# Performance work log

Hardware: AMD Instinct MI355X
Metric: run time of the kernel (lower is better)

Reference implementation:

```python
import jax, jax.numpy as jnp
import numpy as np

BS, FH, FW, NA = 32, 100, 100, 9
IMG_H, IMG_W = 1600, 1600
STRIDE = 16
KEEP_PRE, KEEP_POST, NMS_THR = 1000, 300, 0.7


def _grid_anchors():
    scales = np.array([128.0, 256.0, 512.0])
    ratios = np.array([0.5, 1.0, 2.0])
    ws, hs = [], []
    for s in scales:
        for r in ratios:
            ws.append(s * np.sqrt(1.0 / r))
            hs.append(s * np.sqrt(r))
    ws, hs = np.array(ws), np.array(hs)  # [9]
    sx = (np.arange(FW) + 0.5) * STRIDE
    sy = (np.arange(FH) + 0.5) * STRIDE
    cx, cy = np.meshgrid(sx, sy)  # [FH,FW]
    cx = cx.reshape(-1, 1)
    cy = cy.reshape(-1, 1)
    anchors = np.stack([
        cx - 0.5 * ws, cy - 0.5 * hs, cx + 0.5 * ws, cy + 0.5 * hs
    ], axis=-1).reshape(-1, 4)  # [FH*FW*NA, 4]
    return anchors.astype(np.float32)


def setup_inputs() -> dict:
    key = jax.random.key(0)
    k1, k2 = jax.random.split(key)
    N = FH * FW * NA
    cls_logits = jax.random.normal(k1, (BS, N, 1), dtype=jnp.float32)
    reg_deltas = jax.random.normal(k2, (BS, N, 4), dtype=jnp.float32) * 0.3
    anchors = jnp.asarray(_grid_anchors())
    return {"cls_logits": cls_logits, "reg_deltas": reg_deltas,
            "anchors": anchors, "img_h": IMG_H, "img_w": IMG_W}


def _offsets2boxes(deltas, anchors):
    # deltas: [bs,N,4] (dx,dy,dw,dh); anchors: [N,4] xyxy
    aw = anchors[:, 2] - anchors[:, 0]
    ah = anchors[:, 3] - anchors[:, 1]
    acx = anchors[:, 0] + 0.5 * aw
    acy = anchors[:, 1] + 0.5 * ah
    cx = deltas[..., 0] * aw + acx
    cy = deltas[..., 1] * ah + acy
    w = jnp.exp(deltas[..., 2]) * aw
    h = jnp.exp(deltas[..., 3]) * ah
    return jnp.stack([cx - 0.5 * w, cy - 0.5 * h, cx + 0.5 * w, cy + 0.5 * h], axis=-1)


def _iou_matrix(b):
    # b: [K,4] -> [K,K]
    area = (b[:, 2] - b[:, 0]) * (b[:, 3] - b[:, 1])
    lt = jnp.maximum(b[:, None, :2], b[None, :, :2])
    rb = jnp.minimum(b[:, None, 2:], b[None, :, 2:])
    wh = jnp.clip(rb - lt, 0.0)
    inter = wh[..., 0] * wh[..., 1]
    return inter / (area[:, None] + area[None, :] - inter + 1e-12)


def _detect_single(boxes, scores, img_h, img_w):
    # boxes: [N,4], scores: [N]
    top_scores, idx = jax.lax.top_k(scores, KEEP_PRE)
    b = boxes[idx]  # [K,4], already score-sorted descending
    b = jnp.stack([
        jnp.clip(b[:, 0], 0.0, img_w), jnp.clip(b[:, 1], 0.0, img_h),
        jnp.clip(b[:, 2], 0.0, img_w), jnp.clip(b[:, 3], 0.0, img_h)
    ], axis=-1)
    iou = _iou_matrix(b)  # [K,K]
    K = KEEP_PRE
    cols = jnp.arange(K)

    def body(i, keep):
        # if box i still kept, suppress later boxes with IoU > thr (greedy NMS)
        sup = keep[i] & (iou[i] > NMS_THR) & (cols > i)
        return keep & ~sup

    keep = jax.lax.fori_loop(0, K, body, jnp.ones((K,), dtype=bool))
    # kept boxes first (stable sort preserves descending-score order), take top P
    order = jnp.argsort(~keep, stable=True)[:KEEP_POST]
    valid = keep[order]
    det = jnp.concatenate([b[order], top_scores[order, None]], axis=-1)
    return det * valid[:, None].astype(det.dtype)  # padded rows zeroed


def reference(cls_logits, reg_deltas, anchors, img_h, img_w):
    bs = cls_logits.shape[0]
    scores = jax.nn.sigmoid(cls_logits.reshape(bs, -1))  # [bs,N]
    boxes = _offsets2boxes(reg_deltas.reshape(bs, -1, 4), anchors)  # [bs,N,4]
    fh = jnp.float32(img_h)
    fw = jnp.float32(img_w)
    dets = jax.vmap(lambda b, s: _detect_single(b, s, fh, fw))(boxes, scores)
    return dets  # [bs, KEEP_POST, 5] (xmin,ymin,xmax,ymax,score), zero-padded
```

## Files before the change

### kernel.cpp

```cpp
#include <hip/hip_runtime.h>
#include <stdint.h>

#pragma clang fp contract(off)

#define BS 32
#define NANCH 90000
#define KEEP_PRE 1000
#define KEEP_POST 300
#define NMS_THR 0.7f
#define NBINS 4096
#define CAND_MAX 4096
#define MW 16
#define CNT_STRIDE 32
#define NSLICE 8

typedef unsigned long long u64;
typedef unsigned int u32;

#define HIST_BYTES ((size_t)BS * NBINS * 4)
#define CNT_OFF    (HIST_BYTES)
#define CNT_BYTES  ((size_t)BS * CNT_STRIDE * 4)
#define BTHR_OFF   (CNT_OFF + CNT_BYTES)
#define CAND_OFF   (BTHR_OFF + 128)
#define BOX_OFF    (CAND_OFF + (size_t)BS * CAND_MAX * 8)
#define SCORE_OFF  (BOX_OFF + (size_t)BS * KEEP_PRE * 16)
#define MASK_OFF   (SCORE_OFF + (size_t)BS * KEEP_PRE * 4)

__device__ __forceinline__ u32 fmono(float f) {
    u32 u = __float_as_uint(f);
    return (u & 0x80000000u) ? ~u : (u | 0x80000000u);
}

__global__ __launch_bounds__(256) void hist_kernel(const float* __restrict__ logits,
                                                   u32* __restrict__ hist) {
    __shared__ u32 lh[NBINS];
    const int b = blockIdx.y;
    for (int i = threadIdx.x; i < NBINS; i += 256) lh[i] = 0;
    __syncthreads();
    const float* src = logits + (size_t)b * NANCH;
    const int stride = 256 * gridDim.x;
    for (int i = blockIdx.x * 256 + threadIdx.x; i < NANCH; i += stride) {
        u32 m = fmono(src[i]);
        atomicAdd(&lh[m >> 20], 1u);
    }
    __syncthreads();
    u32* gh = hist + (size_t)b * NBINS;
    for (int i = threadIdx.x; i < NBINS; i += 256)
        if (lh[i]) atomicAdd(&gh[i], lh[i]);
}

__global__ __launch_bounds__(256) void thresh_kernel(const u32* __restrict__ hist,
                                                     u32* __restrict__ Bthr) {
    __shared__ u32 part[256];
    const int b = blockIdx.x;
    const u32* h = hist + (size_t)b * NBINS;
    u32 s = 0;
    for (int k = 0; k < 16; k++) s += h[threadIdx.x * 16 + k];
    part[threadIdx.x] = s;
    __syncthreads();
    if (threadIdx.x == 0) {
        u32 cum = 0;
        int c = 255;
        for (; c >= 0; c--) {
            if (cum + part[c] >= KEEP_PRE) break;
            cum += part[c];
        }
        if (c < 0) c = 0;
        int bin = c * 16 + 15;
        for (; bin >= c * 16; bin--) {
            if (cum + h[bin] >= KEEP_PRE) break;
            cum += h[bin];
        }
        if (bin < c * 16) bin = c * 16;
        Bthr[b] = (u32)bin;
    }
}

__global__ __launch_bounds__(256) void compact_kernel(const float* __restrict__ logits,
                                                      const u32* __restrict__ Bthr,
                                                      u32* __restrict__ cnt,
                                                      u64* __restrict__ cand) {
    const int b = blockIdx.y;
    const int i = blockIdx.x * 256 + threadIdx.x;
    __shared__ u32 blk_cnt;
    __shared__ u32 blk_base;
    if (threadIdx.x == 0) blk_cnt = 0;
    __syncthreads();
    bool is_cand = false;
    u32 m = 0;
    if (i < NANCH) {
        m = fmono(logits[(size_t)b * NANCH + i]);
        is_cand = (m >> 20) >= Bthr[b];
    }
    u64 ballot = __ballot(is_cand);
    const u32 lane = threadIdx.x & 63;
    u32 wbase = 0;
    u32 old = 0;
    if (ballot) {
        if (lane == 0) old = atomicAdd(&blk_cnt, (u32)__popcll(ballot));
        wbase = __shfl(old, 0);
    }
    __syncthreads();
    if (threadIdx.x == 0 && blk_cnt)
        blk_base = atomicAdd(&cnt[b * CNT_STRIDE], blk_cnt);
    __syncthreads();
    if (is_cand) {
        u32 prefix = (u32)__popcll(ballot & ((1ull << lane) - 1ull));
        u32 pos = blk_base + wbase + prefix;
        if (pos < CAND_MAX)
            cand[(size_t)b * CAND_MAX + pos] = ((u64)m << 32) | (u32)(~(u32)i);
    }
}

__global__ __launch_bounds__(256) void select_kernel(const float* __restrict__ deltas,
                                                     const float* __restrict__ anchors,
                                                     const u32* __restrict__ cnt,
                                                     const u64* __restrict__ cand,
                                                     float4* __restrict__ selbox,
                                                     float* __restrict__ selscore,
                                                     const int* __restrict__ p_img_h,
                                                     const int* __restrict__ p_img_w) {
    __shared__ u64 keys[CAND_MAX];
    const int b = blockIdx.y;
    const int slice = blockIdx.x;
    const int n = (int)min(cnt[b * CNT_STRIDE], (u32)CAND_MAX);
    const u64* src = cand + (size_t)b * CAND_MAX;
    for (int i = threadIdx.x; i < n; i += 256)
        keys[i] = src[i];
    __syncthreads();
    const int per = (n + NSLICE - 1) / NSLICE;
    const int i0 = slice * per;
    const int i1 = min(i0 + per, n);
    const float W = (float)(*p_img_w);
    const float H = (float)(*p_img_h);
    const float4* d4 = (const float4*)deltas;
    const float4* a4 = (const float4*)anchors;
    for (int i = i0 + threadIdx.x; i < i1; i += 256) {
        const u64 me = keys[i];
        int rank = 0;
        int j = 0;
        for (; j + 16 <= n; j += 16) {
            int r0 = 0;
#pragma unroll
            for (int k = 0; k < 16; k++) r0 += (keys[j + k] > me);
            rank += r0;
        }
        for (; j < n; j++) rank += (keys[j] > me);
        if (rank < KEEP_PRE) {
            u32 idx = ~(u32)me;
            u32 m = (u32)(me >> 32);
            u32 ub = (m & 0x80000000u) ? (m ^ 0x80000000u) : ~m;
            float logit = __uint_as_float(ub);
            float score = 1.0f / (1.0f + expf(-logit));
            float4 d = d4[(size_t)b * NANCH + idx];
            float4 a = a4[idx];
            float aw = a.z - a.x, ah = a.w - a.y;
            float acx = a.x + 0.5f * aw, acy = a.y + 0.5f * ah;
            float cx = d.x * aw + acx, cy = d.y * ah + acy;
            float w = expf(d.z) * aw, h = expf(d.w) * ah;
            float x1 = cx - 0.5f * w, y1 = cy - 0.5f * h;
            float x2 = cx + 0.5f * w, y2 = cy + 0.5f * h;
            x1 = fminf(fmaxf(x1, 0.0f), W); y1 = fminf(fmaxf(y1, 0.0f), H);
            x2 = fminf(fmaxf(x2, 0.0f), W); y2 = fminf(fmaxf(y2, 0.0f), H);
            selbox[(size_t)b * KEEP_PRE + rank] = make_float4(x1, y1, x2, y2);
            selscore[(size_t)b * KEEP_PRE + rank] = score;
        }
    }
}

__global__ __launch_bounds__(256) void iou_kernel(const float4* __restrict__ selbox,
                                                  u64* __restrict__ mask) {
    const int b = blockIdx.y;
    const int w = blockIdx.x & 15;
    const int chunk = blockIdx.x >> 4;
    const int i = chunk * 256 + threadIdx.x;
    __shared__ float4 cb[64];
    __shared__ float ca[64];
    if (threadIdx.x < 64) {
        int j = w * 64 + threadIdx.x;
        float4 bx = (j < KEEP_PRE) ? selbox[(size_t)b * KEEP_PRE + j]
                                   : make_float4(0, 0, 0, 0);
        cb[threadIdx.x] = bx;
        ca[threadIdx.x] = (bx.z - bx.x) * (bx.w - bx.y);
    }
    __syncthreads();
    if (i >= KEEP_PRE) return;
    float4 bi = selbox[(size_t)b * KEEP_PRE + i];
    float ai = (bi.z - bi.x) * (bi.w - bi.y);
    u64 bits = 0;
    const int jbase = w * 64;
    for (int jj = 0; jj < 64; jj++) {
        int j = jbase + jj;
        if (j > i && j < KEEP_PRE) {
            float4 bj = cb[jj];
            float ltx = fmaxf(bi.x, bj.x), lty = fmaxf(bi.y, bj.y);
            float rbx = fminf(bi.z, bj.z), rby = fminf(bi.w, bj.w);
            float wx = fmaxf(rbx - ltx, 0.0f), wy = fmaxf(rby - lty, 0.0f);
            float inter = wx * wy;
            float denom = ai + ca[jj] - inter + 1e-12f;
            if (inter / denom > NMS_THR) bits |= (1ull << jj);
        }
    }
    mask[((size_t)b * KEEP_PRE + i) * MW + w] = bits;
}

#define CH_ROWS 64
#define CH_WORDS (CH_ROWS * MW)
#define NCHUNK ((KEEP_PRE + CH_ROWS - 1) / CH_ROWS)

__global__ __launch_bounds__(256) void nms_out_kernel(const u64* __restrict__ mask,
                                                      const float4* __restrict__ selbox,
                                                      const float* __restrict__ selscore,
                                                      float* __restrict__ out) {
    const int b = blockIdx.x;
    __shared__ u64 lbuf[2][CH_WORDS];
    __shared__ u64 keepw[MW];
    __shared__ u32 wpre[MW + 1];
    __shared__ int ls_stop;
    const int tid = threadIdx.x;
    const u64* mrow = mask + (size_t)b * KEEP_PRE * MW;

    auto load_chunk = [&](int c) {
        int idx = tid - 128;
        if (idx < 0) return;
        const int words = (c == NCHUNK - 1)
                            ? (KEEP_PRE - (NCHUNK - 1) * CH_ROWS) * MW
                            : CH_WORDS;
        const u64* gsrc = mrow + (size_t)c * CH_WORDS;
        u64* dst = lbuf[c & 1];
#pragma unroll
        for (int k = 0; k < 4; k++) {
            int off = k * 256 + idx * 2;
            ulonglong2 v;
            if (off < words) v = *(const ulonglong2*)(gsrc + off);
            else { v.x = 0ull; v.y = 0ull; }
            *(ulonglong2*)(dst + off) = v;
        }
    };

    if (tid == 0) ls_stop = 0;
    load_chunk(0);
    __syncthreads();

    u64 remv = 0;
    int kept_total = 0;
    const int lw = tid & 15;
    for (int c = 0; c < NCHUNK; c++) {
        if (c + 1 < NCHUNK) load_chunk(c + 1);
        if (tid < 64) {
            const u64* lb = lbuf[c & 1];
            u64 cur = __shfl(remv, c);
#pragma unroll
            for (int blk = 0; blk < 8; blk++) {
                u64 R[8], rwv[8];
#pragma unroll
                for (int k = 0; k < 8; k++)
                    R[k] = lb[(size_t)(blk * 8 + k) * MW + lw];
#pragma unroll
                for (int k = 0; k < 8; k++)
                    rwv[k] = lb[(size_t)(blk * 8 + k) * MW + c];
#pragma unroll
                for (int k = 0; k < 8; k++) {
                    const int p = blk * 8 + k;
                    u64 msk = ((cur >> p) & 1ull) ? 0ull : ~0ull;
                    remv |= R[k] & msk;
                    cur  |= rwv[k] & msk;
                }
            }
            kept_total += 64 - (int)__popcll(cur);
            if (c + 1 < NCHUNK && kept_total >= KEEP_POST) {
                if (lw > c) remv = ~0ull;
                if (tid == 0) ls_stop = 1;
            }
        }
        __syncthreads();
        if (ls_stop) break;
    }

    if (tid < MW) {
        u64 kw = ~remv;
        if (tid == MW - 1) kw &= (1ull << (KEEP_PRE - 64 * (MW - 1))) - 1ull;
        keepw[tid] = kw;
    }
    __syncthreads();
    if (tid == 0) {
        u32 cnt = 0;
        for (int w = 0; w < MW; w++) { wpre[w] = cnt; cnt += (u32)__popcll(keepw[w]); }
        wpre[MW] = cnt;
    }
    __syncthreads();
    const int total = (int)wpre[MW];
    float* outb = out + (size_t)b * KEEP_POST * 5;
    for (int i = tid; i < KEEP_PRE; i += 256) {
        int w = i >> 6;
        u64 kw = keepw[w];
        if ((kw >> (i & 63)) & 1ull) {
            int rank = (int)wpre[w] + __popcll(kw & ((1ull << (i & 63)) - 1ull));
            if (rank < KEEP_POST) {
                float4 bx = selbox[(size_t)b * KEEP_PRE + i];
                float sc = selscore[(size_t)b * KEEP_PRE + i];
                outb[rank * 5 + 0] = bx.x;
                outb[rank * 5 + 1] = bx.y;
                outb[rank * 5 + 2] = bx.z;
                outb[rank * 5 + 3] = bx.w;
                outb[rank * 5 + 4] = sc;
            }
        }
    }
    for (int r = tid; r < KEEP_POST; r += 256) {
        if (r >= total) {
            outb[r * 5 + 0] = 0.0f;
            outb[r * 5 + 1] = 0.0f;
            outb[r * 5 + 2] = 0.0f;
            outb[r * 5 + 3] = 0.0f;
            outb[r * 5 + 4] = 0.0f;
        }
    }
}

extern "C" void kernel_launch(void* const* d_in, const int* in_sizes, int n_in,
                              void* d_out, int out_size, void* d_ws, size_t ws_size,
                              hipStream_t stream) {
    const float* logits  = (const float*)d_in[0];
    const float* deltas  = (const float*)d_in[1];
    const float* anchors = (const float*)d_in[2];
    const int* p_img_h   = (const int*)d_in[3];
    const int* p_img_w   = (const int*)d_in[4];

    char* ws = (char*)d_ws;
    u32* hist     = (u32*)(ws);
    u32* cnt      = (u32*)(ws + CNT_OFF);
    u32* Bthr     = (u32*)(ws + BTHR_OFF);
    u64* cand     = (u64*)(ws + CAND_OFF);
    float4* selbox = (float4*)(ws + BOX_OFF);
    float* selscore = (float*)(ws + SCORE_OFF);
    u64* mask     = (u64*)(ws + MASK_OFF);

    hipMemsetAsync(ws, 0, CNT_OFF + CNT_BYTES, stream);

    hist_kernel<<<dim3(16, BS), 256, 0, stream>>>(logits, hist);
    thresh_kernel<<<BS, 256, 0, stream>>>(hist, Bthr);
    compact_kernel<<<dim3((NANCH + 255) / 256, BS), 256, 0, stream>>>(logits, Bthr, cnt, cand);
    select_kernel<<<dim3(NSLICE, BS), 256, 0, stream>>>(deltas, anchors, cnt, cand,
                                                        selbox, selscore, p_img_h, p_img_w);
    iou_kernel<<<dim3(64, BS), 256, 0, stream>>>(selbox, mask);
    nms_out_kernel<<<BS, 256, 0, stream>>>(mask, selbox, selscore, (float*)d_out);
}
```

Before: 187.0 us.

## Fuse RPN proposal pipeline into a single cooperative kernel with grid syncs

Replaces the memset and six separate kernel launches (histogram, threshold, compaction, rank-select, IoU mask, NMS/output) with one cooperative kernel of 256 blocks that uses grid.sync between stages. This removes per-launch overhead and inter-kernel gaps, and the stages share a union of shared-memory buffers. In exchange, the compaction and IoU stages now run on 256 blocks instead of thousands, serialising more work per block. Grid-wide barriers also carry their own cost, and several stages leave most blocks idle.

```diff
diff --git a/kernel.cpp b/kernel.cpp
--- a/kernel.cpp
+++ b/kernel.cpp
@@ -1,5 +1,8 @@
 #include <hip/hip_runtime.h>
+#include <hip/hip_cooperative_groups.h>
 #include <stdint.h>
+
+namespace cg = cooperative_groups;
 
 #pragma clang fp contract(off)
 
@@ -13,6 +16,7 @@
 #define MW 16
 #define CNT_STRIDE 32
 #define NSLICE 8
+#define SLICE_N 11250
 
 typedef unsigned long long u64;
 typedef unsigned int u32;
@@ -26,294 +30,310 @@
 #define SCORE_OFF  (BOX_OFF + (size_t)BS * KEEP_PRE * 16)
 #define MASK_OFF   (SCORE_OFF + (size_t)BS * KEEP_PRE * 4)
 
+#define CH_ROWS 64
+#define CH_WORDS (CH_ROWS * MW)
+#define NCHUNK ((KEEP_PRE + CH_ROWS - 1) / CH_ROWS)
+
 __device__ __forceinline__ u32 fmono(float f) {
     u32 u = __float_as_uint(f);
     return (u & 0x80000000u) ? ~u : (u | 0x80000000u);
 }
 
-__global__ __launch_bounds__(256) void hist_kernel(const float* __restrict__ logits,
-                                                   u32* __restrict__ hist) {
-    __shared__ u32 lh[NBINS];
-    const int b = blockIdx.y;
-    for (int i = threadIdx.x; i < NBINS; i += 256) lh[i] = 0;
-    __syncthreads();
-    const float* src = logits + (size_t)b * NANCH;
-    const int stride = 256 * gridDim.x;
-    for (int i = blockIdx.x * 256 + threadIdx.x; i < NANCH; i += stride) {
-        u32 m = fmono(src[i]);
-        atomicAdd(&lh[m >> 20], 1u);
-    }
-    __syncthreads();
-    u32* gh = hist + (size_t)b * NBINS;
-    for (int i = threadIdx.x; i < NBINS; i += 256)
-        if (lh[i]) atomicAdd(&gh[i], lh[i]);
-}
-
-__global__ __launch_bounds__(256) void thresh_kernel(const u32* __restrict__ hist,
-                                                     u32* __restrict__ Bthr) {
-    __shared__ u32 part[256];
-    const int b = blockIdx.x;
-    const u32* h = hist + (size_t)b * NBINS;
-    u32 s = 0;
-    for (int k = 0; k < 16; k++) s += h[threadIdx.x * 16 + k];
-    part[threadIdx.x] = s;
-    __syncthreads();
-    if (threadIdx.x == 0) {
-        u32 cum = 0;
-        int c = 255;
-        for (; c >= 0; c--) {
-            if (cum + part[c] >= KEEP_PRE) break;
-            cum += part[c];
-        }
-        if (c < 0) c = 0;
-        int bin = c * 16 + 15;
-        for (; bin >= c * 16; bin--) {
-            if (cum + h[bin] >= KEEP_PRE) break;
-            cum += h[bin];
-        }
-        if (bin < c * 16) bin = c * 16;
-        Bthr[b] = (u32)bin;
-    }
-}
-
-__global__ __launch_bounds__(256) void compact_kernel(const float* __restrict__ logits,
-                                                      const u32* __restrict__ Bthr,
-                                                      u32* __restrict__ cnt,
-                                                      u64* __restrict__ cand) {
-    const int b = blockIdx.y;
-    const int i = blockIdx.x * 256 + threadIdx.x;
-    __shared__ u32 blk_cnt;
-    __shared__ u32 blk_base;
-    if (threadIdx.x == 0) blk_cnt = 0;
-    __syncthreads();
-    bool is_cand = false;
-    u32 m = 0;
-    if (i < NANCH) {
-        m = fmono(logits[(size_t)b * NANCH + i]);
-        is_cand = (m >> 20) >= Bthr[b];
-    }
-    u64 ballot = __ballot(is_cand);
-    const u32 lane = threadIdx.x & 63;
-    u32 wbase = 0;
-    u32 old = 0;
-    if (ballot) {
-        if (lane == 0) old = atomicAdd(&blk_cnt, (u32)__popcll(ballot));
-        wbase = __shfl(old, 0);
-    }
-    __syncthreads();
-    if (threadIdx.x == 0 && blk_cnt)
-        blk_base = atomicAdd(&cnt[b * CNT_STRIDE], blk_cnt);
-    __syncthreads();
-    if (is_cand) {
-        u32 prefix = (u32)__popcll(ballot & ((1ull << lane) - 1ull));
-        u32 pos = blk_base + wbase + prefix;
-        if (pos < CAND_MAX)
-            cand[(size_t)b * CAND_MAX + pos] = ((u64)m << 32) | (u32)(~(u32)i);
-    }
-}
-
-__global__ __launch_bounds__(256) void select_kernel(const float* __restrict__ deltas,
-                                                     const float* __restrict__ anchors,
-                                                     const u32* __restrict__ cnt,
-                                                     const u64* __restrict__ cand,
-                                                     float4* __restrict__ selbox,
-                                                     float* __restrict__ selscore,
-                                                     const int* __restrict__ p_img_h,
-                                                     const int* __restrict__ p_img_w) {
-    __shared__ u64 keys[CAND_MAX];
-    const int b = blockIdx.y;
-    const int slice = blockIdx.x;
-    const int n = (int)min(cnt[b * CNT_STRIDE], (u32)CAND_MAX);
-    const u64* src = cand + (size_t)b * CAND_MAX;
-    for (int i = threadIdx.x; i < n; i += 256)
-        keys[i] = src[i];
-    __syncthreads();
-    const int per = (n + NSLICE - 1) / NSLICE;
-    const int i0 = slice * per;
-    const int i1 = min(i0 + per, n);
-    const float W = (float)(*p_img_w);
-    const float H = (float)(*p_img_h);
-    const float4* d4 = (const float4*)deltas;
-    const float4* a4 = (const float4*)anchors;
-    for (int i = i0 + threadIdx.x; i < i1; i += 256) {
-        const u64 me = keys[i];
-        int rank = 0;
-        int j = 0;
-        for (; j + 16 <= n; j += 16) {
-            int r0 = 0;
-#pragma unroll
-            for (int k = 0; k < 16; k++) r0 += (keys[j + k] > me);
-            rank += r0;
-        }
-        for (; j < n; j++) rank += (keys[j] > me);
-        if (rank < KEEP_PRE) {
-            u32 idx = ~(u32)me;
-            u32 m = (u32)(me >> 32);
-            u32 ub = (m & 0x80000000u) ? (m ^ 0x80000000u) : ~m;
-            float logit = __uint_as_float(ub);
-            float score = 1.0f / (1.0f + expf(-logit));
-            float4 d = d4[(size_t)b * NANCH + idx];
-            float4 a = a4[idx];
-            float aw = a.z - a.x, ah = a.w - a.y;
-            float acx = a.x + 0.5f * aw, acy = a.y + 0.5f * ah;
-            float cx = d.x * aw + acx, cy = d.y * ah + acy;
-            float w = expf(d.z) * aw, h = expf(d.w) * ah;
-            float x1 = cx - 0.5f * w, y1 = cy - 0.5f * h;
-            float x2 = cx + 0.5f * w, y2 = cy + 0.5f * h;
-            x1 = fminf(fmaxf(x1, 0.0f), W); y1 = fminf(fmaxf(y1, 0.0f), H);
-            x2 = fminf(fmaxf(x2, 0.0f), W); y2 = fminf(fmaxf(y2, 0.0f), H);
-            selbox[(size_t)b * KEEP_PRE + rank] = make_float4(x1, y1, x2, y2);
-            selscore[(size_t)b * KEEP_PRE + rank] = score;
-        }
-    }
-}
-
-__global__ __launch_bounds__(256) void iou_kernel(const float4* __restrict__ selbox,
-                                                  u64* __restrict__ mask) {
-    const int b = blockIdx.y;
-    const int w = blockIdx.x & 15;
-    const int chunk = blockIdx.x >> 4;
-    const int i = chunk * 256 + threadIdx.x;
-    __shared__ float4 cb[64];
-    __shared__ float ca[64];
-    if (threadIdx.x < 64) {
-        int j = w * 64 + threadIdx.x;
-        float4 bx = (j < KEEP_PRE) ? selbox[(size_t)b * KEEP_PRE + j]
-                                   : make_float4(0, 0, 0, 0);
-        cb[threadIdx.x] = bx;
-        ca[threadIdx.x] = (bx.z - bx.x) * (bx.w - bx.y);
-    }
-    __syncthreads();
-    if (i >= KEEP_PRE) return;
-    float4 bi = selbox[(size_t)b * KEEP_PRE + i];
-    float ai = (bi.z - bi.x) * (bi.w - bi.y);
-    u64 bits = 0;
-    const int jbase = w * 64;
-    for (int jj = 0; jj < 64; jj++) {
-        int j = jbase + jj;
-        if (j > i && j < KEEP_PRE) {
-            float4 bj = cb[jj];
-            float ltx = fmaxf(bi.x, bj.x), lty = fmaxf(bi.y, bj.y);
-            float rbx = fminf(bi.z, bj.z), rby = fminf(bi.w, bj.w);
-            float wx = fmaxf(rbx - ltx, 0.0f), wy = fmaxf(rby - lty, 0.0f);
-            float inter = wx * wy;
-            float denom = ai + ca[jj] - inter + 1e-12f;
-            if (inter / denom > NMS_THR) bits |= (1ull << jj);
-        }
-    }
-    mask[((size_t)b * KEEP_PRE + i) * MW + w] = bits;
-}
-
-#define CH_ROWS 64
-#define CH_WORDS (CH_ROWS * MW)
-#define NCHUNK ((KEEP_PRE + CH_ROWS - 1) / CH_ROWS)
-
-__global__ __launch_bounds__(256) void nms_out_kernel(const u64* __restrict__ mask,
-                                                      const float4* __restrict__ selbox,
-                                                      const float* __restrict__ selscore,
-                                                      float* __restrict__ out) {
-    const int b = blockIdx.x;
-    __shared__ u64 lbuf[2][CH_WORDS];
-    __shared__ u64 keepw[MW];
-    __shared__ u32 wpre[MW + 1];
-    __shared__ int ls_stop;
+struct NmsSm { u64 lbuf[2][CH_WORDS]; u64 keepw[MW]; u32 wpre[MW + 1]; int stop; };
+struct IouSm { float4 cb[64]; float ca[64]; };
+union SMem {
+    u32 hist[NBINS];
+    u32 part[256];
+    u64 keys[CAND_MAX];
+    IouSm iou;
+    NmsSm nms;
+};
+
+__global__ __launch_bounds__(256) void fused_kernel(
+        const float* __restrict__ logits, const float* __restrict__ deltas,
+        const float* __restrict__ anchors, const int* __restrict__ p_img_h,
+        const int* __restrict__ p_img_w, u32* __restrict__ hist,
+        u32* __restrict__ cnt, u32* __restrict__ Bthr, u64* __restrict__ cand,
+        float4* __restrict__ selbox, float* __restrict__ selscore,
+        u64* __restrict__ mask, float* __restrict__ out) {
+    cg::grid_group grid = cg::this_grid();
+    __shared__ SMem sm;
+    const int blk = blockIdx.x;
     const int tid = threadIdx.x;
-    const u64* mrow = mask + (size_t)b * KEEP_PRE * MW;
-
-    auto load_chunk = [&](int c) {
-        int idx = tid - 128;
-        if (idx < 0) return;
-        const int words = (c == NCHUNK - 1)
-                            ? (KEEP_PRE - (NCHUNK - 1) * CH_ROWS) * MW
-                            : CH_WORDS;
-        const u64* gsrc = mrow + (size_t)c * CH_WORDS;
-        u64* dst = lbuf[c & 1];
-#pragma unroll
-        for (int k = 0; k < 4; k++) {
-            int off = k * 256 + idx * 2;
-            ulonglong2 v;
-            if (off < words) v = *(const ulonglong2*)(gsrc + off);
-            else { v.x = 0ull; v.y = 0ull; }
-            *(ulonglong2*)(dst + off) = v;
-        }
-    };
-
-    if (tid == 0) ls_stop = 0;
-    load_chunk(0);
-    __syncthreads();
-
-    u64 remv = 0;
-    int kept_total = 0;
-    const int lw = tid & 15;
-    for (int c = 0; c < NCHUNK; c++) {
-        if (c + 1 < NCHUNK) load_chunk(c + 1);
-        if (tid < 64) {
-            const u64* lb = lbuf[c & 1];
-            u64 cur = __shfl(remv, c);
-#pragma unroll
-            for (int blk = 0; blk < 8; blk++) {
-                u64 R[8], rwv[8];
-#pragma unroll
-                for (int k = 0; k < 8; k++)
-                    R[k] = lb[(size_t)(blk * 8 + k) * MW + lw];
-#pragma unroll
-                for (int k = 0; k < 8; k++)
-                    rwv[k] = lb[(size_t)(blk * 8 + k) * MW + c];
-#pragma unroll
-                for (int k = 0; k < 8; k++) {
-                    const int p = blk * 8 + k;
-                    u64 msk = ((cur >> p) & 1ull) ? 0ull : ~0ull;
-                    remv |= R[k] & msk;
-                    cur  |= rwv[k] & msk;
-                }
-            }
-            kept_total += 64 - (int)__popcll(cur);
-            if (c + 1 < NCHUNK && kept_total >= KEEP_POST) {
-                if (lw > c) remv = ~0ull;
-                if (tid == 0) ls_stop = 1;
-            }
-        }
-        __syncthreads();
-        if (ls_stop) break;
-    }
-
-    if (tid < MW) {
-        u64 kw = ~remv;
-        if (tid == MW - 1) kw &= (1ull << (KEEP_PRE - 64 * (MW - 1))) - 1ull;
-        keepw[tid] = kw;
-    }
-    __syncthreads();
-    if (tid == 0) {
-        u32 cnt = 0;
-        for (int w = 0; w < MW; w++) { wpre[w] = cnt; cnt += (u32)__popcll(keepw[w]); }
-        wpre[MW] = cnt;
-    }
-    __syncthreads();
-    const int total = (int)wpre[MW];
-    float* outb = out + (size_t)b * KEEP_POST * 5;
-    for (int i = tid; i < KEEP_PRE; i += 256) {
-        int w = i >> 6;
-        u64 kw = keepw[w];
-        if ((kw >> (i & 63)) & 1ull) {
-            int rank = (int)wpre[w] + __popcll(kw & ((1ull << (i & 63)) - 1ull));
-            if (rank < KEEP_POST) {
-                float4 bx = selbox[(size_t)b * KEEP_PRE + i];
-                float sc = selscore[(size_t)b * KEEP_PRE + i];
-                outb[rank * 5 + 0] = bx.x;
-                outb[rank * 5 + 1] = bx.y;
-                outb[rank * 5 + 2] = bx.z;
-                outb[rank * 5 + 3] = bx.w;
-                outb[rank * 5 + 4] = sc;
-            }
-        }
-    }
-    for (int r = tid; r < KEEP_POST; r += 256) {
-        if (r >= total) {
-            outb[r * 5 + 0] = 0.0f;
-            outb[r * 5 + 1] = 0.0f;
-            outb[r * 5 + 2] = 0.0f;
-            outb[r * 5 + 3] = 0.0f;
-            outb[r * 5 + 4] = 0.0f;
+    const int b = blk >> 3;
+    const int slice = blk & 7;
+    const int gtid = blk * 256 + tid;
+    const int gsize = 256 * 256;
+
+    for (int i = gtid; i < BS * NBINS; i += gsize) hist[i] = 0;
+    for (int i = gtid; i < BS * CNT_STRIDE; i += gsize) cnt[i] = 0;
+    grid.sync();
+
+    {
+        for (int i = tid; i < NBINS; i += 256) sm.hist[i] = 0;
+        __syncthreads();
+        const float* src = logits + (size_t)b * NANCH;
+        for (int i = slice * 256 + tid; i < NANCH; i += NSLICE * 256) {
+            u32 m = fmono(src[i]);
+            atomicAdd(&sm.hist[m >> 20], 1u);
+        }
+        __syncthreads();
+        u32* gh = hist + (size_t)b * NBINS;
+        for (int i = tid; i < NBINS; i += 256)
+            if (sm.hist[i]) atomicAdd(&gh[i], sm.hist[i]);
+    }
+    grid.sync();
+
+    if (blk < BS) {
+        const u32* h = hist + (size_t)blk * NBINS;
+        u32 s = 0;
+        for (int k = 0; k < 16; k++)
+            s += __hip_atomic_load(&h[tid * 16 + k], __ATOMIC_RELAXED,
+                                   __HIP_MEMORY_SCOPE_AGENT);
+        sm.part[tid] = s;
+        __syncthreads();
+        if (tid == 0) {
+            u32 cum = 0;
+            int c = 255;
+            for (; c >= 0; c--) {
+                if (cum + sm.part[c] >= KEEP_PRE) break;
+                cum += sm.part[c];
+            }
+            if (c < 0) c = 0;
+            int bin = c * 16 + 15;
+            for (; bin >= c * 16; bin--) {
+                u32 hv = __hip_atomic_load(&h[bin], __ATOMIC_RELAXED,
+                                           __HIP_MEMORY_SCOPE_AGENT);
+                if (cum + hv >= KEEP_PRE) break;
+                cum += hv;
+            }
+            if (bin < c * 16) bin = c * 16;
+            __hip_atomic_store(&Bthr[blk], (u32)bin, __ATOMIC_RELEASE,
+                               __HIP_MEMORY_SCOPE_AGENT);
+        }
+    }
+    grid.sync();
+
+    {
+        const u32 thr = __hip_atomic_load(&Bthr[b], __ATOMIC_ACQUIRE,
+                                          __HIP_MEMORY_SCOPE_AGENT);
+        const float* src = logits + (size_t)b * NANCH;
+        u64* cb_ = cand + (size_t)b * CAND_MAX;
+        u32* pc = &cnt[b * CNT_STRIDE];
+        const int base0 = slice * SLICE_N;
+        const u32 lane = tid & 63;
+        for (int it = 0; it < SLICE_N; it += 256) {
+            int r = it + tid;
+            bool is_cand = false;
+            u32 m = 0;
+            if (r < SLICE_N) {
+                m = fmono(src[base0 + r]);
+                is_cand = (m >> 20) >= thr;
+            }
+            u64 ballot = __ballot(is_cand);
+            if (ballot) {
+                u32 old = 0;
+                if (lane == 0) old = atomicAdd(pc, (u32)__popcll(ballot));
+                u32 wb = __shfl(old, 0);
+                if (is_cand) {
+                    u32 prefix = (u32)__popcll(ballot & ((1ull << lane) - 1ull));
+                    u32 pos = wb + prefix;
+                    if (pos < CAND_MAX)
+                        cb_[pos] = ((u64)m << 32) | (u32)(~(u32)(base0 + r));
+                }
+            }
+        }
+    }
+    grid.sync();
+
+    {
+        const int n = (int)min(
+            __hip_atomic_load(&cnt[b * CNT_STRIDE], __ATOMIC_ACQUIRE,
+                              __HIP_MEMORY_SCOPE_AGENT), (u32)CAND_MAX);
+        const u64* src = cand + (size_t)b * CAND_MAX;
+        for (int i = tid; i < n; i += 256) sm.keys[i] = src[i];
+        __syncthreads();
+        const int per = (n + NSLICE - 1) / NSLICE;
+        const int i0 = slice * per;
+        const int i1 = min(i0 + per, n);
+        const float W = (float)(*p_img_w);
+        const float H = (float)(*p_img_h);
+        const float4* d4 = (const float4*)deltas;
+        const float4* a4 = (const float4*)anchors;
+        for (int i = i0 + tid; i < i1; i += 256) {
+            const u64 me = sm.keys[i];
+            int rank = 0;
+            int j = 0;
+            for (; j + 16 <= n; j += 16) {
+                int r0 = 0;
+#pragma unroll
+                for (int k = 0; k < 16; k++) r0 += (sm.keys[j + k] > me);
+                rank += r0;
+            }
+            for (; j < n; j++) rank += (sm.keys[j] > me);
+            if (rank < KEEP_PRE) {
+                u32 idx = ~(u32)me;
+                u32 m = (u32)(me >> 32);
+                u32 ub = (m & 0x80000000u) ? (m ^ 0x80000000u) : ~m;
+                float logit = __uint_as_float(ub);
+                float score = 1.0f / (1.0f + expf(-logit));
+                float4 d = d4[(size_t)b * NANCH + idx];
+                float4 a = a4[idx];
+                float aw = a.z - a.x, ah = a.w - a.y;
+                float acx = a.x + 0.5f * aw, acy = a.y + 0.5f * ah;
+                float cx = d.x * aw + acx, cy = d.y * ah + acy;
+                float w = expf(d.z) * aw, h = expf(d.w) * ah;
+                float x1 = cx - 0.5f * w, y1 = cy - 0.5f * h;
+                float x2 = cx + 0.5f * w, y2 = cy + 0.5f * h;
+                x1 = fminf(fmaxf(x1, 0.0f), W); y1 = fminf(fmaxf(y1, 0.0f), H);
+                x2 = fminf(fmaxf(x2, 0.0f), W); y2 = fminf(fmaxf(y2, 0.0f), H);
+                selbox[(size_t)b * KEEP_PRE + rank] = make_float4(x1, y1, x2, y2);
+                selscore[(size_t)b * KEEP_PRE + rank] = score;
+            }
+        }
+    }
+    grid.sync();
+
+    {
+#pragma unroll
+        for (int w2 = 0; w2 < 2; w2++) {
+            const int w = slice * 2 + w2;
+            __syncthreads();
+            if (tid < 64) {
+                int j = w * 64 + tid;
+                float4 bx = (j < KEEP_PRE) ? selbox[(size_t)b * KEEP_PRE + j]
+                                           : make_float4(0, 0, 0, 0);
+                sm.iou.cb[tid] = bx;
+                sm.iou.ca[tid] = (bx.z - bx.x) * (bx.w - bx.y);
+            }
+            __syncthreads();
+            const int jbase = w * 64;
+            for (int i = tid; i < KEEP_PRE; i += 256) {
+                float4 bi = selbox[(size_t)b * KEEP_PRE + i];
+                float ai = (bi.z - bi.x) * (bi.w - bi.y);
+                u64 bits = 0;
+                for (int jj = 0; jj < 64; jj++) {
+                    int j = jbase + jj;
+                    if (j > i && j < KEEP_PRE) {
+                        float4 bj = sm.iou.cb[jj];
+                        float ltx = fmaxf(bi.x, bj.x), lty = fmaxf(bi.y, bj.y);
+                        float rbx = fminf(bi.z, bj.z), rby = fminf(bi.w, bj.w);
+                        float wx = fmaxf(rbx - ltx, 0.0f), wy = fmaxf(rby - lty, 0.0f);
+                        float inter = wx * wy;
+                        float denom = ai + sm.iou.ca[jj] - inter + 1e-12f;
+                        if (inter / denom > NMS_THR) bits |= (1ull << jj);
+                    }
+                }
+                mask[((size_t)b * KEEP_PRE + i) * MW + w] = bits;
+            }
+        }
+    }
+    grid.sync();
+
+    if (blk < BS) {
+        const int ib = blk;
+        const u64* mrow = mask + (size_t)ib * KEEP_PRE * MW;
+
+        auto load_chunk = [&](int c) {
+            int idx = tid - 128;
+            if (idx < 0) return;
+            const int words = (c == NCHUNK - 1)
+                                ? (KEEP_PRE - (NCHUNK - 1) * CH_ROWS) * MW
+                                : CH_WORDS;
+            const u64* gsrc = mrow + (size_t)c * CH_WORDS;
+            u64* dst = sm.nms.lbuf[c & 1];
+#pragma unroll
+            for (int k = 0; k < 4; k++) {
+                int off = k * 256 + idx * 2;
+                ulonglong2 v;
+                if (off < words) v = *(const ulonglong2*)(gsrc + off);
+                else { v.x = 0ull; v.y = 0ull; }
+                *(ulonglong2*)(dst + off) = v;
+            }
+        };
+
+        if (tid == 0) sm.nms.stop = 0;
+        __syncthreads();
+        load_chunk(0);
+        __syncthreads();
+
+        u64 remv = 0;
+        int kept_total = 0;
+        const int lw = tid & 15;
+        for (int c = 0; c < NCHUNK; c++) {
+            if (c + 1 < NCHUNK) load_chunk(c + 1);
+            if (tid < 64) {
+                const u64* lb = sm.nms.lbuf[c & 1];
+                u64 cur = __shfl(remv, c);
+#pragma unroll
+                for (int blk8 = 0; blk8 < 8; blk8++) {
+                    u64 R[8], rwv[8];
+#pragma unroll
+                    for (int k = 0; k < 8; k++)
+                        R[k] = lb[(size_t)(blk8 * 8 + k) * MW + lw];
+#pragma unroll
+                    for (int k = 0; k < 8; k++)
+                        rwv[k] = lb[(size_t)(blk8 * 8 + k) * MW + c];
+#pragma unroll
+                    for (int k = 0; k < 8; k++) {
+                        const int p = blk8 * 8 + k;
+                        u64 msk = ((cur >> p) & 1ull) ? 0ull : ~0ull;
+                        remv |= R[k] & msk;
+                        cur  |= rwv[k] & msk;
+                    }
+                }
+                kept_total += 64 - (int)__popcll(cur);
+                if (c + 1 < NCHUNK && kept_total >= KEEP_POST) {
+                    if (lw > c) remv = ~0ull;
+                    if (tid == 0) sm.nms.stop = 1;
+                }
+            }
+            __syncthreads();
+            if (sm.nms.stop) break;
+        }
+
+        if (tid < MW) {
+            u64 kw = ~remv;
+            if (tid == MW - 1) kw &= (1ull << (KEEP_PRE - 64 * (MW - 1))) - 1ull;
+            sm.nms.keepw[tid] = kw;
+        }
+        __syncthreads();
+        if (tid == 0) {
+            u32 c2 = 0;
+            for (int w = 0; w < MW; w++) {
+                sm.nms.wpre[w] = c2;
+                c2 += (u32)__popcll(sm.nms.keepw[w]);
+            }
+            sm.nms.wpre[MW] = c2;
+        }
+        __syncthreads();
+        const int total = (int)sm.nms.wpre[MW];
+        float* outb = out + (size_t)ib * KEEP_POST * 5;
+        for (int i = tid; i < KEEP_PRE; i += 256) {
+            int w = i >> 6;
+            u64 kw = sm.nms.keepw[w];
+            if ((kw >> (i & 63)) & 1ull) {
+                int rank = (int)sm.nms.wpre[w]
+                         + __popcll(kw & ((1ull << (i & 63)) - 1ull));
+                if (rank < KEEP_POST) {
+                    float4 bx = selbox[(size_t)ib * KEEP_PRE + i];
+                    float sc = selscore[(size_t)ib * KEEP_PRE + i];
+                    outb[rank * 5 + 0] = bx.x;
+                    outb[rank * 5 + 1] = bx.y;
+                    outb[rank * 5 + 2] = bx.z;
+                    outb[rank * 5 + 3] = bx.w;
+                    outb[rank * 5 + 4] = sc;
+                }
+            }
+        }
+        for (int r = tid; r < KEEP_POST; r += 256) {
+            if (r >= total) {
+                outb[r * 5 + 0] = 0.0f;
+                outb[r * 5 + 1] = 0.0f;
+                outb[r * 5 + 2] = 0.0f;
+                outb[r * 5 + 3] = 0.0f;
+                outb[r * 5 + 4] = 0.0f;
+            }
         }
     }
 }
@@ -328,21 +348,21 @@
     const int* p_img_w   = (const int*)d_in[4];
 
     char* ws = (char*)d_ws;
-    u32* hist     = (u32*)(ws);
-    u32* cnt      = (u32*)(ws + CNT_OFF);
-    u32* Bthr     = (u32*)(ws + BTHR_OFF);
-    u64* cand     = (u64*)(ws + CAND_OFF);
+    u32* hist      = (u32*)(ws);
+    u32* cnt       = (u32*)(ws + CNT_OFF);
+    u32* Bthr      = (u32*)(ws + BTHR_OFF);
+    u64* cand      = (u64*)(ws + CAND_OFF);
     float4* selbox = (float4*)(ws + BOX_OFF);
     float* selscore = (float*)(ws + SCORE_OFF);
-    u64* mask     = (u64*)(ws + MASK_OFF);
-
-    hipMemsetAsync(ws, 0, CNT_OFF + CNT_BYTES, stream);
-
-    hist_kernel<<<dim3(16, BS), 256, 0, stream>>>(logits, hist);
-    thresh_kernel<<<BS, 256, 0, stream>>>(hist, Bthr);
-    compact_kernel<<<dim3((NANCH + 255) / 256, BS), 256, 0, stream>>>(logits, Bthr, cnt, cand);
-    select_kernel<<<dim3(NSLICE, BS), 256, 0, stream>>>(deltas, anchors, cnt, cand,
-                                                        selbox, selscore, p_img_h, p_img_w);
-    iou_kernel<<<dim3(64, BS), 256, 0, stream>>>(selbox, mask);
-    nms_out_kernel<<<BS, 256, 0, stream>>>(mask, selbox, selscore, (float*)d_out);
+    u64* mask      = (u64*)(ws + MASK_OFF);
+    float* outp    = (float*)d_out;
+
+    void* args[] = {
+        (void*)&logits, (void*)&deltas, (void*)&anchors,
+        (void*)&p_img_h, (void*)&p_img_w,
+        (void*)&hist, (void*)&cnt, (void*)&Bthr, (void*)&cand,
+        (void*)&selbox, (void*)&selscore, (void*)&mask, (void*)&outp
+    };
+    hipLaunchCooperativeKernel((const void*)fused_kernel,
+                               dim3(BS * NSLICE), dim3(256), args, 0, stream);
 }
```

Measured after the change: 428.4 us. +129.1%, slower.
